# Performance work log

Measured on AMD Instinct MI355X. Metric: run time of the kernel, lower is better.

The kernel has to match this reference:

```python
import jax, jax.numpy as jnp
import numpy as np

B, C, W = 8, 128, 4096
REDUCTION = 8
D = C // REDUCTION  # 16


def setup_inputs() -> dict:
    key = jax.random.key(0)
    ks = jax.random.split(key, 7)
    scale = 0.05
    return {
        "x": jax.random.normal(ks[0], (B, C, W), dtype=jnp.float32),
        "Wq": jax.random.normal(ks[1], (D, C), dtype=jnp.float32) * scale,
        "bq": jax.random.normal(ks[2], (D,), dtype=jnp.float32) * scale,
        "Wk": jax.random.normal(ks[3], (D, C), dtype=jnp.float32) * scale,
        "bk": jax.random.normal(ks[4], (D,), dtype=jnp.float32) * scale,
        "Wv": jax.random.normal(ks[5], (C, C), dtype=jnp.float32) * scale,
        "bv": jax.random.normal(ks[6], (C,), dtype=jnp.float32) * scale,
    }


def reference(x, Wq, bq, Wk, bk, Wv, bv):
    # 1x1 Conv1d == per-position linear over channel axis
    q = jnp.einsum('dc,bcw->bdw', Wq, x) + bq[None, :, None]   # [B, D, W]
    k = jnp.einsum('dc,bcw->bdw', Wk, x) + bk[None, :, None]   # [B, D, W]
    v = jnp.einsum('oc,bcw->bow', Wv, x) + bv[None, :, None]   # [B, C, W]
    scale = D ** (-0.5)
    # scores[b,i,j] = q[b,:,i] . k[b,:,j]
    scores = jnp.einsum('bdi,bdj->bij', q, k) * scale          # [B, W, W]
    attn = jax.nn.softmax(scores, axis=-1)
    # torch.bmm(value, attn): context[b,c,w] = sum_j v[b,c,j] * attn[b,j,w]
    context = jnp.einsum('bcj,bjw->bcw', v, attn)              # [B, C, W]
    return context + x
```

## Files before the change

kernel.cpp:

```cpp
#include <hip/hip_runtime.h>

#define B_ 8
#define C_ 128
#define W_ 4096
#define D_ 16
#define SCALE2 0.3606737602222409f

typedef short bf16x8 __attribute__((ext_vector_type(8)));
typedef float f32x4 __attribute__((ext_vector_type(4)));

__device__ __forceinline__ unsigned short f2bf(float f) {
    unsigned int u = __float_as_uint(f);
    u += 0x7fffu + ((u >> 16) & 1u);
    return (unsigned short)(u >> 16);
}
__device__ __forceinline__ unsigned int pk2bf(float lo, float hi) {
    return __builtin_amdgcn_perm(__float_as_uint(hi), __float_as_uint(lo), 0x07060302u);
}
__device__ __forceinline__ bf16x8 u4_to_bf8(unsigned int a, unsigned int b,
                                            unsigned int c, unsigned int d) {
    union { uint4 u; bf16x8 v; } t;
    t.u = make_uint4(a, b, c, d);
    return t.v;
}
__device__ __forceinline__ bf16x8 exp2pack(f32x4 a, f32x4 b) {
    return u4_to_bf8(
        pk2bf(__builtin_amdgcn_exp2f(a[0]), __builtin_amdgcn_exp2f(a[1])),
        pk2bf(__builtin_amdgcn_exp2f(a[2]), __builtin_amdgcn_exp2f(a[3])),
        pk2bf(__builtin_amdgcn_exp2f(b[0]), __builtin_amdgcn_exp2f(b[1])),
        pk2bf(__builtin_amdgcn_exp2f(b[2]), __builtin_amdgcn_exp2f(b[3])));
}
__device__ __forceinline__ int xswz(int j, int c8) {
    return c8 ^ (j & 7) ^ ((j >> 3) & 7);
}

__global__ __launch_bounds__(256) void prep(
    const float* __restrict__ Wq, const float* __restrict__ Wk, const float* __restrict__ Wv,
    unsigned short* __restrict__ Wvbf, unsigned short* __restrict__ Wqkbf)
{
    int g = blockIdx.x * 256 + threadIdx.x;
    const float* src; unsigned short* dst; float sc = 1.0f;
    if (g < 4096)      { src = Wv + g * 4;            dst = Wvbf + g * 4; }
    else if (g < 4608) { int t = g - 4096; src = Wq + t * 4; dst = Wqkbf + t * 4; sc = SCALE2; }
    else               { int t = g - 4608; src = Wk + t * 4; dst = Wqkbf + 2048 + t * 4; }
    float4 v = *(const float4*)src;
    unsigned short h[4] = {f2bf(v.x * sc), f2bf(v.y * sc), f2bf(v.z * sc), f2bf(v.w * sc)};
    *(ushort4*)dst = *(ushort4*)h;
}

__global__ __launch_bounds__(256) void proj(
    const float* __restrict__ x, const unsigned short* __restrict__ Wvbf,
    const unsigned short* __restrict__ Wqkbf,
    const float* __restrict__ bqp, const float* __restrict__ bkp, const float* __restrict__ bvp,
    unsigned short* __restrict__ qws, unsigned short* __restrict__ kws,
    unsigned short* __restrict__ vws)
{
    __shared__ unsigned short xbf[32 * 128];
    __shared__ unsigned short outs[128 * 40];

    int b  = blockIdx.x & 7;
    int j0 = (blockIdx.x >> 3) * 32;
    int tid = threadIdx.x;
    int wid = tid >> 6, lane = tid & 63, n = lane & 15, q4 = lane >> 4;

    {
        unsigned int* xbf32 = (unsigned int*)xbf;
#pragma unroll
        for (int i = 0; i < 8; i++) {
            int p = tid + 256 * i;
            int c2 = p >> 5;
            int j  = p & 31;
            const float* xp = x + (size_t)(b * C_ + 2 * c2) * W_ + j0 + j;
            float lo = xp[0];
            float hi = xp[W_];
            xbf32[j * 64 + xswz(j, c2 >> 2) * 4 + (c2 & 3)] = pk2bf(lo, hi);
        }
    }
    __syncthreads();

    const f32x4 zero = {0.f, 0.f, 0.f, 0.f};
    f32x4 accv[2][2]; f32x4 accqk = zero;
#pragma unroll
    for (int os = 0; os < 2; os++)
#pragma unroll
        for (int js = 0; js < 2; js++) accv[os][js] = zero;

    int isK = wid >> 1;
    int jsm = wid & 1;

#pragma unroll
    for (int kk = 0; kk < 128; kk += 32) {
        bf16x8 av[2], aqkf, bx[2];
#pragma unroll
        for (int os = 0; os < 2; os++)
            av[os] = *(const bf16x8*)(Wvbf + (wid * 32 + os * 16 + n) * 128 + kk + q4 * 8);
        aqkf = *(const bf16x8*)(Wqkbf + (isK * 16 + n) * 128 + kk + q4 * 8);
#pragma unroll
        for (int js = 0; js < 2; js++) {
            int j = js * 16 + n;
            bx[js] = *(const bf16x8*)&xbf[j * 128 + xswz(j, (kk >> 3) + q4) * 8];
        }
#pragma unroll
        for (int os = 0; os < 2; os++)
#pragma unroll
            for (int js = 0; js < 2; js++)
                accv[os][js] = __builtin_amdgcn_mfma_f32_16x16x32_bf16(av[os], bx[js], accv[os][js], 0, 0, 0);
        accqk = __builtin_amdgcn_mfma_f32_16x16x32_bf16(aqkf, bx[jsm], accqk, 0, 0, 0);
    }

    {
        int pos = j0 + jsm * 16 + n;
        const float* bias = isK ? bkp : bqp;
        float bsc = isK ? 1.0f : SCALE2;
        float v0 = accqk[0] + bias[q4 * 4 + 0] * bsc;
        float v1 = accqk[1] + bias[q4 * 4 + 1] * bsc;
        float v2 = accqk[2] + bias[q4 * 4 + 2] * bsc;
        float v3 = accqk[3] + bias[q4 * 4 + 3] * bsc;
        unsigned short* basep = isK ? kws : qws;
        size_t base = ((size_t)(b * 4 + (q4 >> 1)) * W_ + pos) * 8 + (q4 & 1) * 4;
        *(uint2*)(basep + base) = make_uint2(pk2bf(v0, v1), pk2bf(v2, v3));
    }
    if (tid < 128) {
        int which = tid >> 6;
        int plane = 2 + ((tid >> 5) & 1);
        int pos = j0 + (tid & 31);
        unsigned short* basep = which ? kws : qws;
        uint4 z = make_uint4(0, 0, 0, 0);
        if (which == 1 && plane == 2) z.x = 0x3f80u;
        *(uint4*)(basep + ((size_t)(b * 4 + plane) * W_ + pos) * 8) = z;
    }

    float bvv[2][4];
#pragma unroll
    for (int os = 0; os < 2; os++)
#pragma unroll
        for (int r = 0; r < 4; r++) bvv[os][r] = bvp[wid * 32 + os * 16 + q4 * 4 + r];
#pragma unroll
    for (int os = 0; os < 2; os++)
#pragma unroll
        for (int js = 0; js < 2; js++)
#pragma unroll
            for (int r = 0; r < 4; r++) {
                int c = wid * 32 + os * 16 + q4 * 4 + r;
                int j = js * 16 + n;
                outs[c * 40 + j] = f2bf(accv[os][js][r] + bvv[os][r]);
            }
    __syncthreads();
    {
        int jt_l = tid >> 7;
        int c    = tid & 127;
        const uint4* src = (const uint4*)&outs[c * 40 + jt_l * 16];
        unsigned short* dst = vws + ((size_t)((b * 256 + (j0 >> 4) + jt_l) * 128 + c)) * 16;
        *(uint4*)(dst + 0) = src[0];
        *(uint4*)(dst + 8) = src[1];
    }
}

__global__ __launch_bounds__(256) void row_stats(
    const unsigned short* __restrict__ qws, const unsigned short* __restrict__ kws,
    float* __restrict__ rlp)
{
    int blk = blockIdx.x;
    int b = blk & 7;
    int j0 = ((blk >> 3) & 63) * 64;
    int wsp = blk >> 9;
    int t0 = wsp * 16;
    int tid = threadIdx.x;
    int wid = tid >> 6, lane = tid & 63, n = lane & 15, q4 = lane >> 4;

    const bf16x8* qbase = (const bf16x8*)qws + (size_t)(b * 4 + q4) * W_;
    const bf16x8* kbase = (const bf16x8*)kws + (size_t)(b * 4 + q4) * W_;
    bf16x8 aq = qbase[j0 + wid * 16 + n];
    const f32x4 zero = {0.f, 0.f, 0.f, 0.f};

    float lt[4] = {0.f, 0.f, 0.f, 0.f};
    bf16x8 k0[4], k1[4];
#pragma unroll
    for (int ws = 0; ws < 4; ws++) {
        k0[ws] = kbase[(t0 + 0) * 64 + ws * 16 + n];
        k1[ws] = kbase[(t0 + 1) * 64 + ws * 16 + n];
    }

#pragma unroll 2
    for (int t = 0; t < 8; t++) {
        f32x4 sa[4], sb[4];
#pragma unroll
        for (int ws = 0; ws < 4; ws++)
            sa[ws] = __builtin_amdgcn_mfma_f32_16x16x32_bf16(aq, k0[ws], zero, 0, 0, 0);
#pragma unroll
        for (int ws = 0; ws < 4; ws++)
            sb[ws] = __builtin_amdgcn_mfma_f32_16x16x32_bf16(aq, k1[ws], zero, 0, 0, 0);
        int ta = t0 + ((2 * t + 2) & 15), tb = t0 + ((2 * t + 3) & 15);
#pragma unroll
        for (int ws = 0; ws < 4; ws++) {
            k0[ws] = kbase[ta * 64 + ws * 16 + n];
            k1[ws] = kbase[tb * 64 + ws * 16 + n];
        }
#pragma unroll
        for (int ws = 0; ws < 4; ws++)
#pragma unroll
            for (int r = 0; r < 4; r++) {
                lt[r] += __builtin_amdgcn_exp2f(sa[ws][r]);
                lt[r] += __builtin_amdgcn_exp2f(sb[ws][r]);
            }
    }
#pragma unroll
    for (int mask = 1; mask < 16; mask <<= 1)
#pragma unroll
        for (int r = 0; r < 4; r++) lt[r] += __shfl_xor(lt[r], mask, 64);
    if (n == 0) {
        f32x4 l4 = {lt[0], lt[1], lt[2], lt[3]};
        *(f32x4*)(rlp + (size_t)wsp * 32768 + (size_t)b * W_ + j0 + wid * 16 + q4 * 4) = l4;
    }
}

__global__ __launch_bounds__(256) void finl(const float* __restrict__ rlp,
                                            unsigned short* __restrict__ qws)
{
    int g = blockIdx.x * 256 + threadIdx.x;
    int b = g >> 12, j = g & (W_ - 1);
    float l = rlp[g] + rlp[32768 + g] + rlp[65536 + g] + rlp[98304 + g];
    qws[((size_t)(b * 4 + 2) * W_ + j) * 8] = f2bf(-__builtin_amdgcn_logf(l));
}

__global__ __launch_bounds__(256, 2) void attn_out(
    const float* __restrict__ x, const unsigned short* __restrict__ qws,
    const unsigned short* __restrict__ kws, const unsigned short* __restrict__ vws,
    float* __restrict__ out)
{
    __shared__ float red[2][128 * 68];

    int b  = blockIdx.x & 7;
    int w0 = (blockIdx.x >> 3) * 64;
    int tid = threadIdx.x;
    int wid = tid >> 6, lane = tid & 63, n = lane & 15, q4 = lane >> 4;

    const bf16x8* qbase = (const bf16x8*)qws + (size_t)(b * 4 + q4) * W_;
    const bf16x8* kbase = (const bf16x8*)kws + (size_t)(b * 4 + q4) * W_;
    const unsigned short* vtb = vws + (size_t)b * 256 * 128 * 16;

    bf16x8 bk[4];
#pragma unroll
    for (int ws = 0; ws < 4; ws++) bk[ws] = kbase[w0 + ws * 16 + n];

    const f32x4 zero = {0.f, 0.f, 0.f, 0.f};
    f32x4 acc[8][4];
#pragma unroll
    for (int mt = 0; mt < 8; mt++)
#pragma unroll
        for (int nt = 0; nt < 4; nt++) acc[mt][nt] = zero;

    bf16x8 aqA = qbase[wid * 16 + n];
    bf16x8 aqB = qbase[64 + wid * 16 + n];
    uint2 vfA[8], vfB[8];
#pragma unroll
    for (int mt = 0; mt < 8; mt++) {
        int c = mt * 16 + n;
        vfA[mt] = *(const uint2*)(vtb + (size_t)((wid) * 128 + c) * 16 + q4 * 4);
        vfB[mt] = *(const uint2*)(vtb + (size_t)((wid + 4) * 128 + c) * 16 + q4 * 4);
    }
    f32x4 sA[4], sB[4];
#pragma unroll
    for (int ws = 0; ws < 4; ws++) {
        sA[ws] = __builtin_amdgcn_mfma_f32_16x16x32_bf16(aqA, bk[ws], zero, 0, 0, 0);
        sB[ws] = __builtin_amdgcn_mfma_f32_16x16x32_bf16(aqB, bk[ws], zero, 0, 0, 0);
    }
    aqA = qbase[128 + wid * 16 + n];
    aqB = qbase[128 + 64 + wid * 16 + n];
    bf16x8 bfrag[4];
#pragma unroll
    for (int ws = 0; ws < 4; ws++) bfrag[ws] = exp2pack(sA[ws], sB[ws]);

    for (int it = 0; it < 32; it++) {
        int itn = (it + 1) & 31;
        uint2 vfA_n[8], vfB_n[8];
        int jtA_n = itn * 8 + wid, jtB_n = jtA_n + 4;
#pragma unroll
        for (int mt = 0; mt < 8; mt++) {
            int c = mt * 16 + n;
            vfA_n[mt] = *(const uint2*)(vtb + (size_t)(jtA_n * 128 + c) * 16 + q4 * 4);
            vfB_n[mt] = *(const uint2*)(vtb + (size_t)(jtB_n * 128 + c) * 16 + q4 * 4);
        }
#pragma unroll
        for (int ws = 0; ws < 4; ws++) {
            sA[ws] = __builtin_amdgcn_mfma_f32_16x16x32_bf16(aqA, bk[ws], zero, 0, 0, 0);
            sB[ws] = __builtin_amdgcn_mfma_f32_16x16x32_bf16(aqB, bk[ws], zero, 0, 0, 0);
        }
        int itn2 = (it + 2) & 31;
        aqA = qbase[itn2 * 128 + wid * 16 + n];
        aqB = qbase[itn2 * 128 + 64 + wid * 16 + n];
#pragma unroll
        for (int mt = 0; mt < 8; mt++) {
            bf16x8 af = u4_to_bf8(vfA[mt].x, vfA[mt].y, vfB[mt].x, vfB[mt].y);
#pragma unroll
            for (int nt = 0; nt < 4; nt++)
                acc[mt][nt] = __builtin_amdgcn_mfma_f32_16x16x32_bf16(af, bfrag[nt], acc[mt][nt], 0, 0, 0);
        }
#pragma unroll
        for (int ws = 0; ws < 4; ws++) bfrag[ws] = exp2pack(sA[ws], sB[ws]);
#pragma unroll
        for (int mt = 0; mt < 8; mt++) { vfA[mt] = vfA_n[mt]; vfB[mt] = vfB_n[mt]; }
    }

    if (wid >= 2) {
        float* buf = red[wid - 2];
#pragma unroll
        for (int mt = 0; mt < 8; mt++)
#pragma unroll
            for (int nt = 0; nt < 4; nt++)
#pragma unroll
                for (int r = 0; r < 4; r++)
                    buf[(mt * 16 + q4 * 4 + r) * 68 + nt * 16 + n] = acc[mt][nt][r];
    }
    __syncthreads();
    if (wid < 2) {
        const float* buf = red[wid];
#pragma unroll
        for (int mt = 0; mt < 8; mt++)
#pragma unroll
            for (int nt = 0; nt < 4; nt++)
#pragma unroll
                for (int r = 0; r < 4; r++)
                    acc[mt][nt][r] += buf[(mt * 16 + q4 * 4 + r) * 68 + nt * 16 + n];
    }
    __syncthreads();
    if (wid == 1) {
        float* buf = red[0];
#pragma unroll
        for (int mt = 0; mt < 8; mt++)
#pragma unroll
            for (int nt = 0; nt < 4; nt++)
#pragma unroll
                for (int r = 0; r < 4; r++)
                    buf[(mt * 16 + q4 * 4 + r) * 68 + nt * 16 + n] = acc[mt][nt][r];
    }
    __syncthreads();
    if (wid == 0) {
        float* buf = red[0];
#pragma unroll
        for (int mt = 0; mt < 8; mt++)
#pragma unroll
            for (int nt = 0; nt < 4; nt++)
#pragma unroll
                for (int r = 0; r < 4; r++) {
                    int idx = (mt * 16 + q4 * 4 + r) * 68 + nt * 16 + n;
                    buf[idx] = acc[mt][nt][r] + buf[idx];
                }
    }
    __syncthreads();
    {
#pragma unroll
        for (int u = 0; u < 8; u++) {
            int k = tid + 256 * u;
            int c = k >> 4, wseg = (k & 15) * 4;
            size_t gidx = (size_t)(b * C_ + c) * W_ + w0 + wseg;
            float4 xv = *(const float4*)(x + gidx);
            const float* s = &red[0][c * 68 + wseg];
            float4 o = make_float4(s[0] + xv.x, s[1] + xv.y, s[2] + xv.z, s[3] + xv.w);
            *(float4*)(out + gidx) = o;
        }
    }
}

extern "C" void kernel_launch(void* const* d_in, const int* in_sizes, int n_in,
                              void* d_out, int out_size, void* d_ws, size_t ws_size,
                              hipStream_t stream)
{
    const float* x  = (const float*)d_in[0];
    const float* Wq = (const float*)d_in[1];
    const float* bq = (const float*)d_in[2];
    const float* Wk = (const float*)d_in[3];
    const float* bk = (const float*)d_in[4];
    const float* Wv = (const float*)d_in[5];
    const float* bv = (const float*)d_in[6];
    float* out = (float*)d_out;

    unsigned short* qws  = (unsigned short*)d_ws;
    unsigned short* kws  = qws + (size_t)1048576;
    unsigned short* vws  = kws + (size_t)1048576;
    unsigned short* Wvbf = vws + (size_t)4194304;
    unsigned short* Wqkbf = Wvbf + 16384;
    float* rlp = (float*)(Wqkbf + 4096);

    prep<<<20, 256, 0, stream>>>(Wq, Wk, Wv, Wvbf, Wqkbf);
    proj<<<1024, 256, 0, stream>>>(x, Wvbf, Wqkbf, bq, bk, bv, qws, kws, vws);
    row_stats<<<2048, 256, 0, stream>>>(qws, kws, rlp);
    finl<<<128, 256, 0, stream>>>(rlp, qws);
    attn_out<<<512, 256, 0, stream>>>(x, qws, kws, vws, out);
}
```

Before: 162.7 us.

## Switch attention to 32x32x16 MFMA and fold softmax normalisation into V

Replaces the 16x16x32 MFMA tiles (which padded the D=16 contraction to 32 with zero planes plus a log-sum bias trick) with 32x32x16 bf16 MFMAs matching D exactly, and relayouts q/k/v workspaces to match the new fragment shapes. The softmax denominator is no longer injected as a -log(l) term in q. A new vscale kernel instead multiplies V rows by 1/l before the output GEMM. This halves wasted MFMA work and q/k storage, at the cost of an extra kernel pass over V and an additional bf16 rounding of the scaled V.

```diff
diff --git a/kernel.cpp b/kernel.cpp
--- a/kernel.cpp
+++ b/kernel.cpp
@@ -8,11 +8,15 @@
 
 typedef short bf16x8 __attribute__((ext_vector_type(8)));
 typedef float f32x4 __attribute__((ext_vector_type(4)));
+typedef float f32x16 __attribute__((ext_vector_type(16)));
 
 __device__ __forceinline__ unsigned short f2bf(float f) {
     unsigned int u = __float_as_uint(f);
     u += 0x7fffu + ((u >> 16) & 1u);
     return (unsigned short)(u >> 16);
+}
+__device__ __forceinline__ float bf2f(unsigned short h) {
+    return __uint_as_float(((unsigned int)h) << 16);
 }
 __device__ __forceinline__ unsigned int pk2bf(float lo, float hi) {
     return __builtin_amdgcn_perm(__float_as_uint(hi), __float_as_uint(lo), 0x07060302u);
@@ -23,12 +27,17 @@
     t.u = make_uint4(a, b, c, d);
     return t.v;
 }
-__device__ __forceinline__ bf16x8 exp2pack(f32x4 a, f32x4 b) {
+__device__ __forceinline__ bf16x8 uint4_as_bf8(uint4 u) {
+    union { uint4 u; bf16x8 v; } t;
+    t.u = u;
+    return t.v;
+}
+__device__ __forceinline__ bf16x8 exp2pack8(f32x16 s, int r0) {
     return u4_to_bf8(
-        pk2bf(__builtin_amdgcn_exp2f(a[0]), __builtin_amdgcn_exp2f(a[1])),
-        pk2bf(__builtin_amdgcn_exp2f(a[2]), __builtin_amdgcn_exp2f(a[3])),
-        pk2bf(__builtin_amdgcn_exp2f(b[0]), __builtin_amdgcn_exp2f(b[1])),
-        pk2bf(__builtin_amdgcn_exp2f(b[2]), __builtin_amdgcn_exp2f(b[3])));
+        pk2bf(__builtin_amdgcn_exp2f(s[r0+0]), __builtin_amdgcn_exp2f(s[r0+1])),
+        pk2bf(__builtin_amdgcn_exp2f(s[r0+2]), __builtin_amdgcn_exp2f(s[r0+3])),
+        pk2bf(__builtin_amdgcn_exp2f(s[r0+4]), __builtin_amdgcn_exp2f(s[r0+5])),
+        pk2bf(__builtin_amdgcn_exp2f(s[r0+6]), __builtin_amdgcn_exp2f(s[r0+7])));
 }
 __device__ __forceinline__ int xswz(int j, int c8) {
     return c8 ^ (j & 7) ^ ((j >> 3) & 7);
@@ -52,14 +61,16 @@
     const float* __restrict__ x, const unsigned short* __restrict__ Wvbf,
     const unsigned short* __restrict__ Wqkbf,
     const float* __restrict__ bqp, const float* __restrict__ bkp, const float* __restrict__ bvp,
-    unsigned short* __restrict__ qws, unsigned short* __restrict__ kws,
-    unsigned short* __restrict__ vws)
+    unsigned short* __restrict__ qws2, unsigned short* __restrict__ kws2,
+    unsigned short* __restrict__ vws2)
 {
     __shared__ unsigned short xbf[32 * 128];
-    __shared__ unsigned short outs[128 * 40];
+    __shared__ unsigned short outs[128 * 36];
+    __shared__ unsigned short qk_s[2][32][24];
 
     int b  = blockIdx.x & 7;
     int j0 = (blockIdx.x >> 3) * 32;
+    int jt = j0 >> 5;
     int tid = threadIdx.x;
     int wid = tid >> 6, lane = tid & 63, n = lane & 15, q4 = lane >> 4;
 
@@ -109,25 +120,12 @@
     }
 
     {
-        int pos = j0 + jsm * 16 + n;
+        int pos = jsm * 16 + n;
         const float* bias = isK ? bkp : bqp;
         float bsc = isK ? 1.0f : SCALE2;
-        float v0 = accqk[0] + bias[q4 * 4 + 0] * bsc;
-        float v1 = accqk[1] + bias[q4 * 4 + 1] * bsc;
-        float v2 = accqk[2] + bias[q4 * 4 + 2] * bsc;
-        float v3 = accqk[3] + bias[q4 * 4 + 3] * bsc;
-        unsigned short* basep = isK ? kws : qws;
-        size_t base = ((size_t)(b * 4 + (q4 >> 1)) * W_ + pos) * 8 + (q4 & 1) * 4;
-        *(uint2*)(basep + base) = make_uint2(pk2bf(v0, v1), pk2bf(v2, v3));
-    }
-    if (tid < 128) {
-        int which = tid >> 6;
-        int plane = 2 + ((tid >> 5) & 1);
-        int pos = j0 + (tid & 31);
-        unsigned short* basep = which ? kws : qws;
-        uint4 z = make_uint4(0, 0, 0, 0);
-        if (which == 1 && plane == 2) z.x = 0x3f80u;
-        *(uint4*)(basep + ((size_t)(b * 4 + plane) * W_ + pos) * 8) = z;
+#pragma unroll
+        for (int r = 0; r < 4; r++)
+            qk_s[isK][pos][q4 * 4 + r] = f2bf(accqk[r] + bias[q4 * 4 + r] * bsc);
     }
 
     float bvv[2][4];
@@ -143,89 +141,104 @@
             for (int r = 0; r < 4; r++) {
                 int c = wid * 32 + os * 16 + q4 * 4 + r;
                 int j = js * 16 + n;
-                outs[c * 40 + j] = f2bf(accv[os][js][r] + bvv[os][r]);
+                outs[c * 36 + j] = f2bf(accv[os][js][r] + bvv[os][r]);
             }
     __syncthreads();
-    {
-        int jt_l = tid >> 7;
-        int c    = tid & 127;
-        const uint4* src = (const uint4*)&outs[c * 40 + jt_l * 16];
-        unsigned short* dst = vws + ((size_t)((b * 256 + (j0 >> 4) + jt_l) * 128 + c)) * 16;
-        *(uint4*)(dst + 0) = src[0];
-        *(uint4*)(dst + 8) = src[1];
+
+    if (tid < 128) {
+        int qk = tid >> 6, hh = (tid >> 5) & 1, jl = tid & 31;
+        uint4 v = *(const uint4*)&qk_s[qk][jl][hh * 8];
+        unsigned short* dst = (qk ? kws2 : qws2)
+            + (size_t)(b * 128 + jt) * 512 + hh * 256 + jl * 8;
+        *(uint4*)dst = v;
+    }
+#pragma unroll
+    for (int rep = 0; rep < 2; rep++) {
+        int t = tid + rep * 256;
+        int c = t & 127, sel = t >> 7;
+        int jb = (sel >> 1) * 16 + (sel & 1) * 4;
+        uint2 lo = *(const uint2*)&outs[c * 36 + jb];
+        uint2 hi = *(const uint2*)&outs[c * 36 + jb + 8];
+        *(uint4*)(vws2 + ((size_t)(b * 128 + jt) * 4 + sel) * 1024 + c * 8) =
+            make_uint4(lo.x, lo.y, hi.x, hi.y);
     }
 }
 
 __global__ __launch_bounds__(256) void row_stats(
-    const unsigned short* __restrict__ qws, const unsigned short* __restrict__ kws,
+    const unsigned short* __restrict__ qws2, const unsigned short* __restrict__ kws2,
     float* __restrict__ rlp)
 {
     int blk = blockIdx.x;
     int b = blk & 7;
-    int j0 = ((blk >> 3) & 63) * 64;
-    int wsp = blk >> 9;
-    int t0 = wsp * 16;
+    int j0 = ((blk >> 3) & 31) * 128;
+    int wsp = blk >> 8;
     int tid = threadIdx.x;
-    int wid = tid >> 6, lane = tid & 63, n = lane & 15, q4 = lane >> 4;
-
-    const bf16x8* qbase = (const bf16x8*)qws + (size_t)(b * 4 + q4) * W_;
-    const bf16x8* kbase = (const bf16x8*)kws + (size_t)(b * 4 + q4) * W_;
-    bf16x8 aq = qbase[j0 + wid * 16 + n];
-    const f32x4 zero = {0.f, 0.f, 0.f, 0.f};
-
-    float lt[4] = {0.f, 0.f, 0.f, 0.f};
-    bf16x8 k0[4], k1[4];
-#pragma unroll
-    for (int ws = 0; ws < 4; ws++) {
-        k0[ws] = kbase[(t0 + 0) * 64 + ws * 16 + n];
-        k1[ws] = kbase[(t0 + 1) * 64 + ws * 16 + n];
-    }
-
-#pragma unroll 2
-    for (int t = 0; t < 8; t++) {
-        f32x4 sa[4], sb[4];
-#pragma unroll
-        for (int ws = 0; ws < 4; ws++)
-            sa[ws] = __builtin_amdgcn_mfma_f32_16x16x32_bf16(aq, k0[ws], zero, 0, 0, 0);
-#pragma unroll
-        for (int ws = 0; ws < 4; ws++)
-            sb[ws] = __builtin_amdgcn_mfma_f32_16x16x32_bf16(aq, k1[ws], zero, 0, 0, 0);
-        int ta = t0 + ((2 * t + 2) & 15), tb = t0 + ((2 * t + 3) & 15);
-#pragma unroll
-        for (int ws = 0; ws < 4; ws++) {
-            k0[ws] = kbase[ta * 64 + ws * 16 + n];
-            k1[ws] = kbase[tb * 64 + ws * 16 + n];
+    int wid = tid >> 6, lane = tid & 63, wl = lane & 31, h = lane >> 5;
+
+    const unsigned short* qb = qws2 + (size_t)b * 65536;
+    const unsigned short* kb = kws2 + (size_t)b * 65536;
+    int jt = (j0 >> 5) + wid;
+
+    bf16x8 aq = *(const bf16x8*)(qb + (size_t)jt * 512 + h * 256 + wl * 8);
+    f32x16 zero16 = {0.f,0.f,0.f,0.f,0.f,0.f,0.f,0.f,0.f,0.f,0.f,0.f,0.f,0.f,0.f,0.f};
+
+    float lt[16];
+#pragma unroll
+    for (int r = 0; r < 16; r++) lt[r] = 0.f;
+
+    bf16x8 bkc = *(const bf16x8*)(kb + (size_t)(wsp * 32) * 512 + h * 256 + wl * 8);
+    for (int t = 0; t < 32; t++) {
+        f32x16 s = __builtin_amdgcn_mfma_f32_32x32x16_bf16(aq, bkc, zero16, 0, 0, 0);
+        int tn = wsp * 32 + ((t + 1) & 31);
+        bkc = *(const bf16x8*)(kb + (size_t)tn * 512 + h * 256 + wl * 8);
+#pragma unroll
+        for (int r = 0; r < 16; r++) lt[r] += __builtin_amdgcn_exp2f(s[r]);
+    }
+#pragma unroll
+    for (int mask = 1; mask < 32; mask <<= 1)
+#pragma unroll
+        for (int r = 0; r < 16; r++) lt[r] += __shfl_xor(lt[r], mask, 64);
+    if (wl == 0) {
+#pragma unroll
+        for (int g = 0; g < 4; g++) {
+            f32x4 v = {lt[4*g+0], lt[4*g+1], lt[4*g+2], lt[4*g+3]};
+            *(f32x4*)(rlp + (size_t)wsp * 32768 + (size_t)b * W_ + j0 + wid * 32 + 4 * h + 8 * g) = v;
         }
-#pragma unroll
-        for (int ws = 0; ws < 4; ws++)
-#pragma unroll
-            for (int r = 0; r < 4; r++) {
-                lt[r] += __builtin_amdgcn_exp2f(sa[ws][r]);
-                lt[r] += __builtin_amdgcn_exp2f(sb[ws][r]);
-            }
-    }
-#pragma unroll
-    for (int mask = 1; mask < 16; mask <<= 1)
-#pragma unroll
-        for (int r = 0; r < 4; r++) lt[r] += __shfl_xor(lt[r], mask, 64);
-    if (n == 0) {
-        f32x4 l4 = {lt[0], lt[1], lt[2], lt[3]};
-        *(f32x4*)(rlp + (size_t)wsp * 32768 + (size_t)b * W_ + j0 + wid * 16 + q4 * 4) = l4;
     }
 }
 
 __global__ __launch_bounds__(256) void finl(const float* __restrict__ rlp,
-                                            unsigned short* __restrict__ qws)
+                                            float* __restrict__ rls)
 {
     int g = blockIdx.x * 256 + threadIdx.x;
-    int b = g >> 12, j = g & (W_ - 1);
     float l = rlp[g] + rlp[32768 + g] + rlp[65536 + g] + rlp[98304 + g];
-    qws[((size_t)(b * 4 + 2) * W_ + j) * 8] = f2bf(-__builtin_amdgcn_logf(l));
+    rls[g] = 1.0f / l;
+}
+
+__global__ __launch_bounds__(256) void vscale(unsigned short* __restrict__ vws2,
+                                              const float* __restrict__ rls)
+{
+    int g = blockIdx.x * 256 + threadIdx.x;
+    int hh = (g >> 7) & 1, kf = (g >> 8) & 1, jt = (g >> 9) & 127, b = g >> 16;
+    int jb = jt * 32 + kf * 16 + 4 * hh;
+    const float* rp = rls + (size_t)b * W_ + jb;
+    float4 r0 = *(const float4*)rp;
+    float4 r1 = *(const float4*)(rp + 8);
+    uint4 v = *(const uint4*)(vws2 + (size_t)g * 8);
+    unsigned int o0 = pk2bf(bf2f((unsigned short)(v.x & 0xffffu)) * r0.x,
+                            bf2f((unsigned short)(v.x >> 16))     * r0.y);
+    unsigned int o1 = pk2bf(bf2f((unsigned short)(v.y & 0xffffu)) * r0.z,
+                            bf2f((unsigned short)(v.y >> 16))     * r0.w);
+    unsigned int o2 = pk2bf(bf2f((unsigned short)(v.z & 0xffffu)) * r1.x,
+                            bf2f((unsigned short)(v.z >> 16))     * r1.y);
+    unsigned int o3 = pk2bf(bf2f((unsigned short)(v.w & 0xffffu)) * r1.z,
+                            bf2f((unsigned short)(v.w >> 16))     * r1.w);
+    *(uint4*)(vws2 + (size_t)g * 8) = make_uint4(o0, o1, o2, o3);
 }
 
 __global__ __launch_bounds__(256, 2) void attn_out(
-    const float* __restrict__ x, const unsigned short* __restrict__ qws,
-    const unsigned short* __restrict__ kws, const unsigned short* __restrict__ vws,
+    const float* __restrict__ x, const unsigned short* __restrict__ qws2,
+    const unsigned short* __restrict__ kws2, const unsigned short* __restrict__ vws2,
     float* __restrict__ out)
 {
     __shared__ float red[2][128 * 68];
@@ -233,132 +246,102 @@
     int b  = blockIdx.x & 7;
     int w0 = (blockIdx.x >> 3) * 64;
     int tid = threadIdx.x;
-    int wid = tid >> 6, lane = tid & 63, n = lane & 15, q4 = lane >> 4;
-
-    const bf16x8* qbase = (const bf16x8*)qws + (size_t)(b * 4 + q4) * W_;
-    const bf16x8* kbase = (const bf16x8*)kws + (size_t)(b * 4 + q4) * W_;
-    const unsigned short* vtb = vws + (size_t)b * 256 * 128 * 16;
-
-    bf16x8 bk[4];
-#pragma unroll
-    for (int ws = 0; ws < 4; ws++) bk[ws] = kbase[w0 + ws * 16 + n];
-
-    const f32x4 zero = {0.f, 0.f, 0.f, 0.f};
-    f32x4 acc[8][4];
-#pragma unroll
-    for (int mt = 0; mt < 8; mt++)
-#pragma unroll
-        for (int nt = 0; nt < 4; nt++) acc[mt][nt] = zero;
-
-    bf16x8 aqA = qbase[wid * 16 + n];
-    bf16x8 aqB = qbase[64 + wid * 16 + n];
-    uint2 vfA[8], vfB[8];
-#pragma unroll
-    for (int mt = 0; mt < 8; mt++) {
-        int c = mt * 16 + n;
-        vfA[mt] = *(const uint2*)(vtb + (size_t)((wid) * 128 + c) * 16 + q4 * 4);
-        vfB[mt] = *(const uint2*)(vtb + (size_t)((wid + 4) * 128 + c) * 16 + q4 * 4);
-    }
-    f32x4 sA[4], sB[4];
-#pragma unroll
-    for (int ws = 0; ws < 4; ws++) {
-        sA[ws] = __builtin_amdgcn_mfma_f32_16x16x32_bf16(aqA, bk[ws], zero, 0, 0, 0);
-        sB[ws] = __builtin_amdgcn_mfma_f32_16x16x32_bf16(aqB, bk[ws], zero, 0, 0, 0);
-    }
-    aqA = qbase[128 + wid * 16 + n];
-    aqB = qbase[128 + 64 + wid * 16 + n];
-    bf16x8 bfrag[4];
-#pragma unroll
-    for (int ws = 0; ws < 4; ws++) bfrag[ws] = exp2pack(sA[ws], sB[ws]);
+    int wid = tid >> 6, lane = tid & 63, wl = lane & 31, h = lane >> 5;
+
+    const unsigned short* qb  = qws2 + (size_t)b * 65536;
+    const unsigned short* kb  = kws2 + (size_t)b * 65536;
+    const unsigned short* vtb = vws2 + (size_t)b * 524288;
+
+    bf16x8 bk0 = *(const bf16x8*)(kb + (size_t)((w0 >> 5) + 0) * 512 + h * 256 + wl * 8);
+    bf16x8 bk1 = *(const bf16x8*)(kb + (size_t)((w0 >> 5) + 1) * 512 + h * 256 + wl * 8);
+
+    f32x16 zero16 = {0.f,0.f,0.f,0.f,0.f,0.f,0.f,0.f,0.f,0.f,0.f,0.f,0.f,0.f,0.f,0.f};
+    f32x16 acc[4][2];
+#pragma unroll
+    for (int mt = 0; mt < 4; mt++)
+#pragma unroll
+        for (int nt = 0; nt < 2; nt++) acc[mt][nt] = zero16;
+
+    const int qoff = h * 256 + wl * 8;
+
+    bf16x8 aq = *(const bf16x8*)(qb + (size_t)(wid) * 512 + qoff);
+    uint4 vf[4][2];
+#pragma unroll
+    for (int mt = 0; mt < 4; mt++)
+#pragma unroll
+        for (int kf = 0; kf < 2; kf++)
+            vf[mt][kf] = *(const uint4*)(vtb + (size_t)wid * 4096 + kf * 2048 + h * 1024 + (mt * 32 + wl) * 8);
+    f32x16 s0 = __builtin_amdgcn_mfma_f32_32x32x16_bf16(aq, bk0, zero16, 0, 0, 0);
+    f32x16 s1 = __builtin_amdgcn_mfma_f32_32x32x16_bf16(aq, bk1, zero16, 0, 0, 0);
+    aq = *(const bf16x8*)(qb + (size_t)(4 + wid) * 512 + qoff);
+    bf16x8 bfrag[2][2];
+    bfrag[0][0] = exp2pack8(s0, 0); bfrag[1][0] = exp2pack8(s0, 8);
+    bfrag[0][1] = exp2pack8(s1, 0); bfrag[1][1] = exp2pack8(s1, 8);
 
     for (int it = 0; it < 32; it++) {
-        int itn = (it + 1) & 31;
-        uint2 vfA_n[8], vfB_n[8];
-        int jtA_n = itn * 8 + wid, jtB_n = jtA_n + 4;
-#pragma unroll
-        for (int mt = 0; mt < 8; mt++) {
-            int c = mt * 16 + n;
-            vfA_n[mt] = *(const uint2*)(vtb + (size_t)(jtA_n * 128 + c) * 16 + q4 * 4);
-            vfB_n[mt] = *(const uint2*)(vtb + (size_t)(jtB_n * 128 + c) * 16 + q4 * 4);
-        }
-#pragma unroll
-        for (int ws = 0; ws < 4; ws++) {
-            sA[ws] = __builtin_amdgcn_mfma_f32_16x16x32_bf16(aqA, bk[ws], zero, 0, 0, 0);
-            sB[ws] = __builtin_amdgcn_mfma_f32_16x16x32_bf16(aqB, bk[ws], zero, 0, 0, 0);
-        }
-        int itn2 = (it + 2) & 31;
-        aqA = qbase[itn2 * 128 + wid * 16 + n];
-        aqB = qbase[itn2 * 128 + 64 + wid * 16 + n];
-#pragma unroll
-        for (int mt = 0; mt < 8; mt++) {
-            bf16x8 af = u4_to_bf8(vfA[mt].x, vfA[mt].y, vfB[mt].x, vfB[mt].y);
-#pragma unroll
-            for (int nt = 0; nt < 4; nt++)
-                acc[mt][nt] = __builtin_amdgcn_mfma_f32_16x16x32_bf16(af, bfrag[nt], acc[mt][nt], 0, 0, 0);
-        }
-#pragma unroll
-        for (int ws = 0; ws < 4; ws++) bfrag[ws] = exp2pack(sA[ws], sB[ws]);
-#pragma unroll
-        for (int mt = 0; mt < 8; mt++) { vfA[mt] = vfA_n[mt]; vfB[mt] = vfB_n[mt]; }
-    }
-
-    if (wid >= 2) {
-        float* buf = red[wid - 2];
-#pragma unroll
-        for (int mt = 0; mt < 8; mt++)
-#pragma unroll
-            for (int nt = 0; nt < 4; nt++)
-#pragma unroll
-                for (int r = 0; r < 4; r++)
-                    buf[(mt * 16 + q4 * 4 + r) * 68 + nt * 16 + n] = acc[mt][nt][r];
-    }
-    __syncthreads();
-    if (wid < 2) {
-        const float* buf = red[wid];
-#pragma unroll
-        for (int mt = 0; mt < 8; mt++)
-#pragma unroll
-            for (int nt = 0; nt < 4; nt++)
-#pragma unroll
-                for (int r = 0; r < 4; r++)
-                    acc[mt][nt][r] += buf[(mt * 16 + q4 * 4 + r) * 68 + nt * 16 + n];
-    }
-    __syncthreads();
-    if (wid == 1) {
-        float* buf = red[0];
-#pragma unroll
-        for (int mt = 0; mt < 8; mt++)
-#pragma unroll
-            for (int nt = 0; nt < 4; nt++)
-#pragma unroll
-                for (int r = 0; r < 4; r++)
-                    buf[(mt * 16 + q4 * 4 + r) * 68 + nt * 16 + n] = acc[mt][nt][r];
-    }
-    __syncthreads();
-    if (wid == 0) {
-        float* buf = red[0];
-#pragma unroll
-        for (int mt = 0; mt < 8; mt++)
-#pragma unroll
-            for (int nt = 0; nt < 4; nt++)
-#pragma unroll
-                for (int r = 0; r < 4; r++) {
-                    int idx = (mt * 16 + q4 * 4 + r) * 68 + nt * 16 + n;
-                    buf[idx] = acc[mt][nt][r] + buf[idx];
-                }
-    }
-    __syncthreads();
-    {
-#pragma unroll
-        for (int u = 0; u < 8; u++) {
-            int k = tid + 256 * u;
-            int c = k >> 4, wseg = (k & 15) * 4;
-            size_t gidx = (size_t)(b * C_ + c) * W_ + w0 + wseg;
-            float4 xv = *(const float4*)(x + gidx);
-            const float* s = &red[0][c * 68 + wseg];
-            float4 o = make_float4(s[0] + xv.x, s[1] + xv.y, s[2] + xv.z, s[3] + xv.w);
-            *(float4*)(out + gidx) = o;
-        }
+        int jtn = ((it + 1) & 31) * 4 + wid;
+        uint4 vfn[4][2];
+#pragma unroll
+        for (int mt = 0; mt < 4; mt++)
+#pragma unroll
+            for (int kf = 0; kf < 2; kf++)
+                vfn[mt][kf] = *(const uint4*)(vtb + (size_t)jtn * 4096 + kf * 2048 + h * 1024 + (mt * 32 + wl) * 8);
+#pragma unroll
+        for (int mt = 0; mt < 4; mt++)
+#pragma unroll
+            for (int kf = 0; kf < 2; kf++) {
+                bf16x8 af = uint4_as_bf8(vf[mt][kf]);
+#pragma unroll
+                for (int nt = 0; nt < 2; nt++)
+                    acc[mt][nt] = __builtin_amdgcn_mfma_f32_32x32x16_bf16(af, bfrag[kf][nt], acc[mt][nt], 0, 0, 0);
+            }
+        s0 = __builtin_amdgcn_mfma_f32_32x32x16_bf16(aq, bk0, zero16, 0, 0, 0);
+        s1 = __builtin_amdgcn_mfma_f32_32x32x16_bf16(aq, bk1, zero16, 0, 0, 0);
+        aq = *(const bf16x8*)(qb + (size_t)(((it + 2) & 31) * 4 + wid) * 512 + qoff);
+        bfrag[0][0] = exp2pack8(s0, 0); bfrag[1][0] = exp2pack8(s0, 8);
+        bfrag[0][1] = exp2pack8(s1, 0); bfrag[1][1] = exp2pack8(s1, 8);
+#pragma unroll
+        for (int mt = 0; mt < 4; mt++)
+#pragma unroll
+            for (int kf = 0; kf < 2; kf++) vf[mt][kf] = vfn[mt][kf];
+    }
+
+#define WRITE_TILE(BUF)                                                           \
+    {                                                                             \
+        float* _b = (BUF);                                                        \
+        _Pragma("unroll") for (int mt = 0; mt < 4; mt++)                          \
+        _Pragma("unroll") for (int nt = 0; nt < 2; nt++)                          \
+        _Pragma("unroll") for (int r = 0; r < 16; r++)                            \
+            _b[(mt * 32 + (r & 3) + 8 * (r >> 2) + 4 * h) * 68 + nt * 32 + wl] = acc[mt][nt][r]; \
+    }
+#define ADD_TILE(BUF)                                                             \
+    {                                                                             \
+        const float* _b = (BUF);                                                  \
+        _Pragma("unroll") for (int mt = 0; mt < 4; mt++)                          \
+        _Pragma("unroll") for (int nt = 0; nt < 2; nt++)                          \
+        _Pragma("unroll") for (int r = 0; r < 16; r++)                            \
+            acc[mt][nt][r] += _b[(mt * 32 + (r & 3) + 8 * (r >> 2) + 4 * h) * 68 + nt * 32 + wl]; \
+    }
+    if (wid >= 2) WRITE_TILE(red[wid - 2]);
+    __syncthreads();
+    if (wid < 2) ADD_TILE(red[wid]);
+    __syncthreads();
+    if (wid == 1) WRITE_TILE(red[0]);
+    __syncthreads();
+    if (wid == 0) { ADD_TILE(red[0]); WRITE_TILE(red[0]); }
+    __syncthreads();
+#undef WRITE_TILE
+#undef ADD_TILE
+
+#pragma unroll
+    for (int u = 0; u < 8; u++) {
+        int k = tid + 256 * u;
+        int c = k >> 4, wseg = (k & 15) * 4;
+        size_t gidx = (size_t)(b * C_ + c) * W_ + w0 + wseg;
+        float4 xv = *(const float4*)(x + gidx);
+        const float* s = &red[0][c * 68 + wseg];
+        float4 o = make_float4(s[0] + xv.x, s[1] + xv.y, s[2] + xv.z, s[3] + xv.w);
+        *(float4*)(out + gidx) = o;
     }
 }
 
@@ -375,16 +358,18 @@
     const float* bv = (const float*)d_in[6];
     float* out = (float*)d_out;
 
-    unsigned short* qws  = (unsigned short*)d_ws;
-    unsigned short* kws  = qws + (size_t)1048576;
-    unsigned short* vws  = kws + (size_t)1048576;
-    unsigned short* Wvbf = vws + (size_t)4194304;
+    unsigned short* qws2 = (unsigned short*)d_ws;
+    unsigned short* kws2 = qws2 + (size_t)524288;
+    unsigned short* vws2 = kws2 + (size_t)524288;
+    unsigned short* Wvbf = vws2 + (size_t)4194304;
     unsigned short* Wqkbf = Wvbf + 16384;
     float* rlp = (float*)(Wqkbf + 4096);
+    float* rls = rlp + 131072;
 
     prep<<<20, 256, 0, stream>>>(Wq, Wk, Wv, Wvbf, Wqkbf);
-    proj<<<1024, 256, 0, stream>>>(x, Wvbf, Wqkbf, bq, bk, bv, qws, kws, vws);
-    row_stats<<<2048, 256, 0, stream>>>(qws, kws, rlp);
-    finl<<<128, 256, 0, stream>>>(rlp, qws);
-    attn_out<<<512, 256, 0, stream>>>(x, qws, kws, vws, out);
-}
+    proj<<<1024, 256, 0, stream>>>(x, Wvbf, Wqkbf, bq, bk, bv, qws2, kws2, vws2);
+    row_stats<<<1024, 256, 0, stream>>>(qws2, kws2, rlp);
+    finl<<<128, 256, 0, stream>>>(rlp, rls);
+    vscale<<<2048, 256, 0, stream>>>(vws2, rls);
+    attn_out<<<512, 256, 0, stream>>>(x, qws2, kws2, vws2, out);
+}
```

Result: no change. 162.4 us (-0.1%).
